# Performance work log

Hardware: AMD Instinct MI355X
Metric: run time of the kernel (lower is better)

## Reference

```python
import math
import jax, jax.numpy as jnp
import numpy as np

N = 50000      # nodes
E = 600000     # edges (before self-loops)
D_IN = 64
COND = 32
B = 50         # cond batch; N % B == 0
DT = 128       # dim_t
DH = 128       # dim_h
L = 3          # num GAT layers
FD = 16        # learned_sinusoidal_dim


def setup_inputs() -> dict:
    key = jax.random.key(0)
    ks = jax.random.split(key, 32)
    p = lambda k, shp: (jax.random.normal(k, shp, jnp.float32) * 0.05)
    return {
        "x": jax.random.normal(ks[0], (N, D_IN), jnp.float32),
        "adj": jax.random.randint(ks[1], (2, E), 0, N, dtype=jnp.int32),
        "ef": jax.random.normal(ks[2], (E, 8), jnp.float32),
        "timesteps": jax.random.uniform(ks[3], (N,), jnp.float32) * 1000.0,
        "cond": jax.random.normal(ks[4], (B, COND), jnp.float32),
        # random fourier weights (fixed, not trained in original since is_random=True)
        "fourier_w": jax.random.normal(ks[5], (FD // 2,), jnp.float32),
        # time MLP: Linear(FD+1, DT) -> SiLU -> Linear(DT, DT)
        "tW1": p(ks[6], (FD + 1, DT)), "tb1": p(ks[7], (DT,)),
        "tW2": p(ks[8], (DT, DT)),   "tb2": p(ks[9], (DT,)),
        # conditional projections
        "pxW": p(ks[10], (D_IN, DT)), "pxb": p(ks[11], (DT,)),
        "pcW": p(ks[12], (COND, DT)), "pcb": p(ks[13], (DT,)),
        # stacked GATConv params (all layers 128->128, heads=1)
        "linW": p(ks[14], (L, DT, DH)),   # lin, bias=False
        "attS": p(ks[15], (L, DH)),       # att_src
        "attD": p(ks[16], (L, DH)),       # att_dst
        "gbias": p(ks[17], (L, DH)),      # GATConv bias
        "resW": p(ks[18], (L, DT, DH)),   # residual Linear, bias=False
        # decode MLP
        "dW1": p(ks[19], (DH, DH)), "db1": p(ks[20], (DH,)),
        "dW2": p(ks[21], (DH, 2)),  "db2": p(ks[22], (2,)),
    }


def _gat_layer(h, src, dst, n, linW, attS, attD, gbias, resW):
    # PyG GATConv, heads=1, concat=True, residual=True, add_self_loops already in src/dst
    xl = h @ linW                          # [n, DH]
    a_src = xl @ attS                      # [n]
    a_dst = xl @ attD                      # [n]
    e = jax.nn.leaky_relu(a_src[src] + a_dst[dst], 0.2)   # [E2]
    m = jax.ops.segment_max(e, dst, num_segments=n)
    w = jnp.exp(e - m[dst])
    den = jax.ops.segment_sum(w, dst, num_segments=n)
    alpha = w / den[dst]                   # softmax per destination node
    out = jax.ops.segment_sum(alpha[:, None] * xl[src], dst, num_segments=n)
    return out + gbias + h @ resW


def reference(x, adj, ef, timesteps, cond, fourier_w, tW1, tb1, tW2, tb2,
              pxW, pxb, pcW, pcb, linW, attS, attD, gbias, resW,
              dW1, db1, dW2, db2):
    n = x.shape[0]
    # time embedding: random fourier features, dim = FD + 1
    t = timesteps[:, None]
    freqs = t * fourier_w[None, :] * (2.0 * math.pi)
    four = jnp.concatenate([t, jnp.sin(freqs), jnp.cos(freqs)], axis=-1)
    temb = jax.nn.silu(four @ tW1 + tb1) @ tW2 + tb2
    # conditional projection (cond repeated to match nodes)
    c = jnp.repeat(cond, n // cond.shape[0], axis=0)
    h = (x @ pxW + pxb) + (c @ pcW + pcb) + temb
    # add self-loops once (PyG GATConv default add_self_loops=True)
    loop = jnp.arange(n, dtype=adj.dtype)
    src = jnp.concatenate([adj[0], loop])
    dst = jnp.concatenate([adj[1], loop])
    for l in range(linW.shape[0]):
        h = _gat_layer(h, src, dst, n, linW[l], attS[l], attD[l], gbias[l], resW[l])
        h = jax.nn.gelu(h, approximate=False)
    # decode MLP
    h = jax.nn.gelu(h @ dW1 + db1, approximate=False)
    return h @ dW2 + db2
```

## Files before the change

kernel.cpp:

```cpp
#include <hip/hip_runtime.h>
#include <hip/hip_bf16.h>

#define N_NODES 50000
#define N_EDGES 600000
#define TOT_EDGES (N_EDGES + N_NODES)
#define NPB 1000
#define SCAN_BLK 49

#define PREP_T0 1563
#define PREP_T1 (PREP_T0 + 544)
#define PREP_T2 (PREP_T1 + 3125)
#define PREP_T3 (PREP_T2 + 25)
#define PREP_T4 (PREP_T3 + 3)

typedef __bf16 bf16x8 __attribute__((ext_vector_type(8)));
typedef float f32x4 __attribute__((ext_vector_type(4)));
typedef unsigned short u16x8 __attribute__((ext_vector_type(8)));

__device__ __forceinline__ float gelu_exact(float v){
  return 0.5f * v * (1.f + erff(v * 0.70710678118654752f));
}
__device__ __forceinline__ float silu(float v){
  return v / (1.f + expf(-v));
}
__device__ __forceinline__ unsigned short f2bf(float f){
  unsigned u = __builtin_bit_cast(unsigned, f);
  unsigned r = (u + 0x7FFFu + ((u >> 16) & 1u)) >> 16;
  return (unsigned short)r;
}
__device__ __forceinline__ float bf2f(unsigned short u){
  return __builtin_bit_cast(float, ((unsigned)u) << 16);
}

__global__ __launch_bounds__(256) void count_deg(const int* __restrict__ adj,
                                                 int* __restrict__ counts,
                                                 int* __restrict__ rank){
  int t = blockIdx.x*256 + threadIdx.x;
  if (t >= N_EDGES/4) return;
  int j4 = t*4;
  const int4 d4 = *(const int4*)&adj[N_EDGES + j4];
  int4 r4;
  r4.x = atomicAdd(&counts[d4.x], 1);
  r4.y = atomicAdd(&counts[d4.y], 1);
  r4.z = atomicAdd(&counts[d4.z], 1);
  r4.w = atomicAdd(&counts[d4.w], 1);
  *(int4*)&rank[j4] = r4;
}

__global__ __launch_bounds__(256) void scan_part(const int* __restrict__ counts, int* __restrict__ blksum){
  int tid = threadIdx.x;
  int base = blockIdx.x*1024 + tid*4;
  int s = 0;
  #pragma unroll
  for (int k = 0; k < 4; k++){ int idx = base+k; if (idx < N_NODES) s += counts[idx] + 1; }
  #pragma unroll
  for (int off = 1; off < 64; off <<= 1) s += __shfl_xor(s, off, 64);
  __shared__ int ws[4];
  int lane = tid & 63, wid = tid >> 6;
  if (lane == 0) ws[wid] = s;
  __syncthreads();
  if (tid == 0) blksum[blockIdx.x] = ws[0]+ws[1]+ws[2]+ws[3];
}

__global__ __launch_bounds__(256) void scan_final(const int* __restrict__ counts,
                                                  const int* __restrict__ blksum,
                                                  int* __restrict__ offsets,
                                                  int* __restrict__ srt_src){
  int tid = threadIdx.x; int lane = tid & 63, wid = tid >> 6;
  __shared__ int ws[4];
  __shared__ int sbase;
  int base = blockIdx.x*1024 + tid*4;
  int v[4]; int s = 0;
  #pragma unroll
  for (int k = 0; k < 4; k++){ int idx = base+k; v[k] = (idx < N_NODES) ? (counts[idx] + 1) : 0; s += v[k]; }
  int x = s;
  #pragma unroll
  for (int off = 1; off < 64; off <<= 1){
    int y = __shfl_up(x, off, 64);
    if (lane >= off) x += y;
  }
  if (lane == 63) ws[wid] = x;
  if (tid < 64){
    int bv = (tid < SCAN_BLK) ? blksum[tid] : 0;
    int bx = bv;
    #pragma unroll
    for (int off = 1; off < 64; off <<= 1){
      int y = __shfl_up(bx, off, 64);
      if (tid >= off) bx += y;
    }
    int basev = (blockIdx.x == 0) ? 0 : __shfl(bx, blockIdx.x - 1, 64);
    int total = __shfl(bx, SCAN_BLK - 1, 64);
    if (tid == 0){
      sbase = basev;
      if (blockIdx.x == SCAN_BLK-1) offsets[N_NODES] = total;
    }
  }
  __syncthreads();
  int run = sbase;
  for (int q = 0; q < wid; q++) run += ws[q];
  run += x - s;
  #pragma unroll
  for (int k = 0; k < 4; k++){
    int idx = base+k;
    if (idx < N_NODES){
      offsets[idx] = run;
      srt_src[run] = idx;
    }
    run += v[k];
  }
}

__global__ __launch_bounds__(256) void scatter_edges(const int* __restrict__ adj,
                                                     const int* __restrict__ rank,
                                                     const int* __restrict__ offsets,
                                                     int* __restrict__ srt_src){
  int t = blockIdx.x*256 + threadIdx.x;
  if (t >= N_EDGES/4) return;
  int j4 = t*4;
  const int4 s4 = *(const int4*)&adj[j4];
  const int4 d4 = *(const int4*)&adj[N_EDGES + j4];
  const int4 r4 = *(const int4*)&rank[j4];
  srt_src[offsets[d4.x] + 1 + r4.x] = s4.x;
  srt_src[offsets[d4.y] + 1 + r4.y] = s4.y;
  srt_src[offsets[d4.z] + 1 + r4.z] = s4.z;
  srt_src[offsets[d4.w] + 1 + r4.w] = s4.w;
}

__global__ __launch_bounds__(256) void prep_all(const float* __restrict__ timesteps,
                                                const float* __restrict__ fw,
                                                const float* __restrict__ tW1,
                                                const float* __restrict__ tb1,
                                                unsigned short* __restrict__ hid,
                                                const float* __restrict__ linW,
                                                const float* __restrict__ resW,
                                                const float* __restrict__ tW2,
                                                const float* __restrict__ pxW,
                                                const float* __restrict__ dW1,
                                                unsigned short* __restrict__ Bt2,
                                                unsigned short* __restrict__ Bt_init,
                                                unsigned short* __restrict__ Bt_d1,
                                                const float* __restrict__ x,
                                                unsigned short* __restrict__ xbf,
                                                const float* __restrict__ cond,
                                                const float* __restrict__ pcW,
                                                const float* __restrict__ pcb,
                                                float* __restrict__ cproj,
                                                const float* __restrict__ attS,
                                                const float* __restrict__ attD,
                                                float* __restrict__ uv){
  __shared__ float sfour[32][17];
  __shared__ float sW[17][128];
  const int bid = blockIdx.x, tid = threadIdx.x;

  if (bid < PREP_T0){
    int row0 = bid * 32;
    if (tid < 32){
      int gr = row0 + tid;
      float t = (gr < N_NODES) ? timesteps[gr] : 0.f;
      sfour[tid][0] = t;
      #pragma unroll
      for (int q = 0; q < 8; q++){
        float f = t * fw[q] * 6.2831853071795864769f;
        float sv, cv;
        sincosf(f, &sv, &cv);
        sfour[tid][1+q] = sv;
        sfour[tid][9+q] = cv;
      }
    }
    for (int i = tid; i < 17*128; i += 256) sW[i>>7][i&127] = tW1[i];
    __syncthreads();
    int j = tid & 127, rg = tid >> 7;
    float b = tb1[j];
    #pragma unroll
    for (int r = 0; r < 16; r++){
      int row = rg*16 + r;
      float acc = b;
      #pragma unroll
      for (int k = 0; k < 17; k++) acc += sfour[row][k]*sW[k][j];
      int gr = row0 + row;
      if (gr < N_NODES) hid[gr*128 + j] = f2bf(silu(acc));
    }
  } else if (bid < PREP_T1){
    int idx = (bid - PREP_T0)*256 + tid;
    if (idx < 98304){
      int j = idx >> 14, e = idx & 16383;
      int l = j >> 1, isres = j & 1;
      int k = e >> 7, c = e & 127;
      const float* src = (isres ? resW : linW) + l*16384;
      Bt2[(size_t)l*32768 + (size_t)(isres*128 + c)*128 + k] = f2bf(src[k*128 + c]);
    } else if (idx < 114688){
      int e = idx - 98304; int k = e >> 7, c = e & 127;
      Bt_init[c*192 + k] = f2bf(tW2[k*128 + c]);
    } else if (idx < 122880){
      int e = idx - 114688; int k = e >> 7, c = e & 127;
      Bt_init[c*192 + 128 + k] = f2bf(pxW[k*128 + c]);
    } else if (idx < 139264){
      int e = idx - 122880; int k = e >> 7, c = e & 127;
      Bt_d1[c*128 + k] = f2bf(dW1[k*128 + c]);
    }
  } else if (bid < PREP_T2){
    int i = (bid - PREP_T1)*256 + tid;
    float4 v = ((const float4*)x)[i];
    ushort4 o;
    o.x = f2bf(v.x); o.y = f2bf(v.y); o.z = f2bf(v.z); o.w = f2bf(v.w);
    *(ushort4*)&xbf[(size_t)i*4] = o;
  } else if (bid < PREP_T3){
    int g = (bid - PREP_T2)*256 + tid;
    int b = g >> 7, j = g & 127;
    float acc = pcb[j];
    for (int k = 0; k < 32; k++) acc += cond[b*32+k]*pcW[k*128+j];
    cproj[b*128+j] = acc;
  } else {
    int g = (bid - PREP_T3)*256 + tid;
    if (g < 768){
      int l = g >> 8, s = (g >> 7) & 1, k = g & 127;
      const float* att = s ? (attD + l*128) : (attS + l*128);
      const float* row = linW + (l*128 + k)*128;
      float acc = 0.f;
      for (int j = 0; j < 128; j++) acc += row[j]*att[j];
      uv[(l*2 + s)*128 + k] = acc;
    }
  }
}

template<int KD, int EPI, bool SWZ, bool DOTS>
__global__ __launch_bounds__(256) void mfma_gemm(const unsigned short* __restrict__ A0,
                                                 const unsigned short* __restrict__ A1,
                                                 const unsigned short* __restrict__ Bt,
                                                 const float* __restrict__ bias0,
                                                 const float* __restrict__ bias1,
                                                 const float* __restrict__ cproj,
                                                 unsigned short* __restrict__ O0,
                                                 unsigned short* __restrict__ O1,
                                                 const float* __restrict__ uv_l,
                                                 float* __restrict__ a_srcO,
                                                 float* __restrict__ a_dstO){
  constexpr int CHR  = KD / 8;
  constexpr int ROWB = KD * 2;
  constexpr int KS   = KD / 32;
  __shared__ alignas(16) char sA[64 * ROWB];
  const int tid  = threadIdx.x;
  int bx, nb;
  if constexpr (SWZ){
    int id = blockIdx.x;
    int nper = gridDim.x >> 3;
    int lin = (id & 7) * nper + (id >> 3);
    bx = lin >> 2; nb = lin & 3;
  } else {
    bx = blockIdx.x; nb = blockIdx.y;
  }
  const int m0   = bx * 64;
  const int lane = tid & 63, w = tid >> 6;
  const int lr   = lane & 15, lk = lane >> 4;

  bf16x8 bfr[4][KS];
  #pragma unroll
  for (int nt = 0; nt < 4; nt++){
    int c = nb*64 + nt*16 + lr;
    #pragma unroll
    for (int ks = 0; ks < KS; ks++)
      bfr[nt][ks] = *(const bf16x8*)&Bt[(size_t)c*KD + ks*32 + lk*8];
  }

  for (int i = tid; i < 64*CHR; i += 256){
    int r = i / CHR, ch = i % CHR;
    int grow = m0 + r;
    u16x8 v;
    #pragma unroll
    for (int q = 0; q < 8; q++) v[q] = 0;
    if (grow < N_NODES){
      if constexpr (KD == 128){
        v = *(const u16x8*)&A0[(size_t)grow*128 + ch*8];
      } else {
        if (ch < 16) v = *(const u16x8*)&A0[(size_t)grow*128 + ch*8];
        else         v = *(const u16x8*)&A1[(size_t)grow*64 + (ch-16)*8];
      }
    }
    *(u16x8*)&sA[r*ROWB + ((ch*16) ^ ((r & 7) << 4))] = v;
  }
  __syncthreads();

  f32x4 acc[4];
  #pragma unroll
  for (int nt = 0; nt < 4; nt++)
    #pragma unroll
    for (int q = 0; q < 4; q++) acc[nt][q] = 0.f;

  const int arow = w*16 + lr;
  #pragma unroll
  for (int ks = 0; ks < KS; ks++){
    bf16x8 a = *(const bf16x8*)&sA[arow*ROWB + ((ks*64 + lk*16) ^ ((arow & 7) << 4))];
    #pragma unroll
    for (int nt = 0; nt < 4; nt++)
      acc[nt] = __builtin_amdgcn_mfma_f32_16x16x32_bf16(a, bfr[nt][ks], acc[nt], 0, 0, 0);
  }

  if constexpr (DOTS){
    if (nb == 0){
      int r = tid >> 2;
      int row = m0 + r;
      if (row < N_NODES){
        float ps = 0.f, pd = 0.f;
        #pragma unroll
        for (int cc = 0; cc < 4; cc++){
          int ch = (tid & 3)*4 + cc;
          u16x8 av = *(const u16x8*)&sA[r*ROWB + ((ch*16) ^ ((r & 7) << 4))];
          int c0 = ch*8;
          const float4 u0 = *(const float4*)&uv_l[c0];
          const float4 u1 = *(const float4*)&uv_l[c0+4];
          const float4 v0 = *(const float4*)&uv_l[128+c0];
          const float4 v1 = *(const float4*)&uv_l[128+c0+4];
          const float uu[8] = {u0.x,u0.y,u0.z,u0.w,u1.x,u1.y,u1.z,u1.w};
          const float vv[8] = {v0.x,v0.y,v0.z,v0.w,v1.x,v1.y,v1.z,v1.w};
          #pragma unroll
          for (int q = 0; q < 8; q++){
            float hv = bf2f(av[q]);
            ps += hv*uu[q];
            pd += hv*vv[q];
          }
        }
        ps += __shfl_xor(ps, 1, 64); ps += __shfl_xor(ps, 2, 64);
        pd += __shfl_xor(pd, 1, 64); pd += __shfl_xor(pd, 2, 64);
        if ((tid & 3) == 0){ a_srcO[row] = ps; a_dstO[row] = pd; }
      }
    }
  }

  const int rbase = m0 + w*16 + lk*4;
  #pragma unroll
  for (int nt = 0; nt < 4; nt++){
    int c = nb*64 + nt*16 + lr;
    #pragma unroll
    for (int rg = 0; rg < 4; rg++){
      int row = rbase + rg;
      if (row >= N_NODES) continue;
      float v = acc[nt][rg];
      if constexpr (EPI == 0){
        if (c < 128) O0[(size_t)row*128 + c]       = f2bf(v);
        else         O1[(size_t)row*128 + (c-128)] = f2bf(v);
      } else if constexpr (EPI == 1){
        v += bias0[c] + bias1[c] + cproj[(row/NPB)*128 + c];
        O0[(size_t)row*128 + c] = f2bf(v);
      } else {
        v = gelu_exact(v + bias0[c]);
        O0[(size_t)row*128 + c] = f2bf(v);
      }
    }
  }
}

template<bool FUSE>
__global__ __launch_bounds__(256) void aggregate(const unsigned short* __restrict__ xl,
                                                 const float* __restrict__ a_src,
                                                 const float* __restrict__ a_dst,
                                                 const unsigned short* __restrict__ hres,
                                                 const float* __restrict__ gbias_l,
                                                 const int* __restrict__ offsets,
                                                 const int* __restrict__ srt_src,
                                                 unsigned short* __restrict__ h_out,
                                                 const float* __restrict__ uv_next,
                                                 float* __restrict__ a_src_o,
                                                 float* __restrict__ a_dst_o){
  const int tid  = threadIdx.x;
  const int lane = tid & 63;
  const int l16  = lane & 15;
  const int i    = blockIdx.x*16 + (tid >> 4);
  const int beg  = offsets[i];
  const int deg  = offsets[i+1] - beg;
  const float adst = a_dst[i];

  int   s0  = 0;
  float ev0 = -INFINITY;
  if (l16 < deg){
    s0 = srt_src[beg + l16];
    float t = a_src[s0] + adst;
    ev0 = (t > 0.f) ? t : 0.2f*t;
  }
  float m = ev0;
  #pragma unroll
  for (int off = 1; off < 16; off <<= 1) m = fmaxf(m, __shfl_xor(m, off, 64));
  float den = (l16 < deg) ? __expf(ev0 - m) : 0.f;
  #pragma unroll
  for (int off = 1; off < 16; off <<= 1) den += __shfl_xor(den, off, 64);
  for (int c0 = 16; c0 < deg; c0 += 16){
    float ev = -INFINITY;
    if (c0 + l16 < deg){
      int s = srt_src[beg + c0 + l16];
      float t = a_src[s] + adst;
      ev = (t > 0.f) ? t : 0.2f*t;
    }
    float cm = ev;
    #pragma unroll
    for (int off = 1; off < 16; off <<= 1) cm = fmaxf(cm, __shfl_xor(cm, off, 64));
    if (cm > m){ den *= __expf(m - cm); m = cm; }
    float wv = (c0 + l16 < deg) ? __expf(ev - m) : 0.f;
    #pragma unroll
    for (int off = 1; off < 16; off <<= 1) wv += __shfl_xor(wv, off, 64);
    den += wv;
  }
  const float inv = 1.f / den;
  float w0 = (l16 < deg) ? __expf(ev0 - m) * inv : 0.f;

  float acc[8];
  #pragma unroll
  for (int k = 0; k < 8; k++) acc[k] = 0.f;
  const int gbb = (lane & 48) << 2;

  int lim0 = deg < 16 ? deg : 16;
  for (int q = 0; q < lim0; q++){
    int addr = gbb + q*4;
    int s    = __builtin_amdgcn_ds_bpermute(addr, s0);
    float wq = __builtin_bit_cast(float, __builtin_amdgcn_ds_bpermute(addr, __builtin_bit_cast(int, w0)));
    const int4 xv = *(const int4*)&xl[((size_t)s << 7) + (l16 << 3)];
    const int xd[4] = {xv.x, xv.y, xv.z, xv.w};
    #pragma unroll
    for (int k = 0; k < 4; k++){
      acc[2*k]   += wq * __builtin_bit_cast(float, xd[k] << 16);
      acc[2*k+1] += wq * __builtin_bit_cast(float, xd[k] & 0xffff0000);
    }
  }
  for (int c0 = 16; c0 < deg; c0 += 16){
    int s1 = 0; float w1 = 0.f;
    if (c0 + l16 < deg){
      s1 = srt_src[beg + c0 + l16];
      float t = a_src[s1] + adst;
      float ev = (t > 0.f) ? t : 0.2f*t;
      w1 = __expf(ev - m) * inv;
    }
    int lim = deg - c0; if (lim > 16) lim = 16;
    for (int q = 0; q < lim; q++){
      int addr = gbb + q*4;
      int s    = __builtin_amdgcn_ds_bpermute(addr, s1);
      float wq = __builtin_bit_cast(float, __builtin_amdgcn_ds_bpermute(addr, __builtin_bit_cast(int, w1)));
      const int4 xv = *(const int4*)&xl[((size_t)s << 7) + (l16 << 3)];
      const int xd[4] = {xv.x, xv.y, xv.z, xv.w};
      #pragma unroll
      for (int k = 0; k < 4; k++){
        acc[2*k]   += wq * __builtin_bit_cast(float, xd[k] << 16);
        acc[2*k+1] += wq * __builtin_bit_cast(float, xd[k] & 0xffff0000);
      }
    }
  }

  const int4 hr = *(const int4*)&hres[((size_t)i << 7) + (l16 << 3)];
  const int hd[4] = {hr.x, hr.y, hr.z, hr.w};
  const float4 gb0 = *(const float4*)&gbias_l[l16*8];
  const float4 gb1 = *(const float4*)&gbias_l[l16*8 + 4];
  const float gbv[8] = {gb0.x, gb0.y, gb0.z, gb0.w, gb1.x, gb1.y, gb1.z, gb1.w};
  float uu[8], vv[8];
  if constexpr (FUSE){
    const float4 a0 = *(const float4*)&uv_next[l16*8];
    const float4 a1 = *(const float4*)&uv_next[l16*8 + 4];
    const float4 b0 = *(const float4*)&uv_next[128 + l16*8];
    const float4 b1 = *(const float4*)&uv_next[128 + l16*8 + 4];
    uu[0]=a0.x; uu[1]=a0.y; uu[2]=a0.z; uu[3]=a0.w; uu[4]=a1.x; uu[5]=a1.y; uu[6]=a1.z; uu[7]=a1.w;
    vv[0]=b0.x; vv[1]=b0.y; vv[2]=b0.z; vv[3]=b0.w; vv[4]=b1.x; vv[5]=b1.y; vv[6]=b1.z; vv[7]=b1.w;
  }
  float ps = 0.f, pd = 0.f;
  int od[4];
  #pragma unroll
  for (int k = 0; k < 4; k++){
    float r0 = acc[2*k]   + gbv[2*k]   + __builtin_bit_cast(float, hd[k] << 16);
    float r1 = acc[2*k+1] + gbv[2*k+1] + __builtin_bit_cast(float, hd[k] & 0xffff0000);
    float g0 = gelu_exact(r0);
    float g1 = gelu_exact(r1);
    if constexpr (FUSE){
      ps += g0*uu[2*k] + g1*uu[2*k+1];
      pd += g0*vv[2*k] + g1*vv[2*k+1];
    }
    unsigned lo = f2bf(g0);
    unsigned hi = f2bf(g1);
    od[k] = (int)(lo | (hi << 16));
  }
  *(int4*)&h_out[((size_t)i << 7) + (l16 << 3)] = make_int4(od[0], od[1], od[2], od[3]);
  if constexpr (FUSE){
    #pragma unroll
    for (int off = 1; off < 16; off <<= 1){
      ps += __shfl_xor(ps, off, 64);
      pd += __shfl_xor(pd, off, 64);
    }
    if (l16 == 0){ a_src_o[i] = ps; a_dst_o[i] = pd; }
  }
}

__global__ __launch_bounds__(256) void head2(const unsigned short* __restrict__ g,
                                             const float* __restrict__ dW2,
                                             const float* __restrict__ db2,
                                             float* __restrict__ out){
  const int tid = threadIdx.x;
  const int l16 = tid & 15;
  const int i   = blockIdx.x*16 + (tid >> 4);
  const int4 gv = *(const int4*)&g[((size_t)i << 7) + (l16 << 3)];
  const int gd[4] = {gv.x, gv.y, gv.z, gv.w};
  float wk[16];
  #pragma unroll
  for (int q = 0; q < 4; q++){
    const float4 wq = *(const float4*)&dW2[l16*16 + q*4];
    wk[q*4+0]=wq.x; wk[q*4+1]=wq.y; wk[q*4+2]=wq.z; wk[q*4+3]=wq.w;
  }
  float p0 = 0.f, p1 = 0.f;
  #pragma unroll
  for (int k = 0; k < 4; k++){
    float lo = __builtin_bit_cast(float, gd[k] << 16);
    float hi = __builtin_bit_cast(float, gd[k] & 0xffff0000);
    p0 += lo*wk[4*k+0] + hi*wk[4*k+2];
    p1 += lo*wk[4*k+1] + hi*wk[4*k+3];
  }
  #pragma unroll
  for (int off = 1; off < 16; off <<= 1){
    p0 += __shfl_xor(p0, off, 64);
    p1 += __shfl_xor(p1, off, 64);
  }
  if (l16 == 0){
    float2 o; o.x = p0 + db2[0]; o.y = p1 + db2[1];
    *(float2*)&out[i*2] = o;
  }
}

extern "C" void kernel_launch(void* const* d_in, const int* in_sizes, int n_in,
                              void* d_out, int out_size, void* d_ws, size_t ws_size,
                              hipStream_t stream) {
  const float* x   = (const float*)d_in[0];
  const int*   adj = (const int*)  d_in[1];
  const float* timesteps = (const float*)d_in[3];
  const float* cond = (const float*)d_in[4];
  const float* fw   = (const float*)d_in[5];
  const float* tW1  = (const float*)d_in[6];
  const float* tb1  = (const float*)d_in[7];
  const float* tW2  = (const float*)d_in[8];
  const float* tb2  = (const float*)d_in[9];
  const float* pxW  = (const float*)d_in[10];
  const float* pxb  = (const float*)d_in[11];
  const float* pcW  = (const float*)d_in[12];
  const float* pcb  = (const float*)d_in[13];
  const float* linW = (const float*)d_in[14];
  const float* attS = (const float*)d_in[15];
  const float* attD = (const float*)d_in[16];
  const float* gbias= (const float*)d_in[17];
  const float* resW = (const float*)d_in[18];
  const float* dW1  = (const float*)d_in[19];
  const float* db1  = (const float*)d_in[20];
  const float* dW2  = (const float*)d_in[21];
  const float* db2  = (const float*)d_in[22];
  float* out = (float*)d_out;

  char* w = (char*)d_ws;
  size_t off = 0;
  auto carve = [&](size_t bytes) -> void* {
    void* p = w + off;
    off = (off + bytes + 255) & ~(size_t)255;
    return p;
  };
  unsigned short* h_bf    = (unsigned short*)carve((size_t)N_NODES*128*2);
  unsigned short* xl_bf   = (unsigned short*)carve((size_t)N_NODES*128*2);
  unsigned short* hres_bf = (unsigned short*)carve((size_t)N_NODES*128*2);
  unsigned short* x_bf    = (unsigned short*)carve((size_t)N_NODES*64*2);
  float* a_src0 = (float*)carve((size_t)N_NODES*4);
  float* a_dst0 = (float*)carve((size_t)N_NODES*4);
  float* a_src1 = (float*)carve((size_t)N_NODES*4);
  float* a_dst1 = (float*)carve((size_t)N_NODES*4);
  float* cproj = (float*)carve(50*128*4);
  float* uv    = (float*)carve(6*128*4);
  int* counts  = (int*)carve((size_t)N_NODES*4);
  int* rank    = (int*)carve((size_t)N_EDGES*4);
  int* offsets = (int*)carve((size_t)(N_NODES+1)*4);
  int* srt_src = (int*)carve((size_t)TOT_EDGES*4);
  int* blksum  = (int*)carve(SCAN_BLK*4);
  unsigned short* Bt2     = (unsigned short*)carve((size_t)3*256*128*2);
  unsigned short* Bt_init = (unsigned short*)carve((size_t)128*192*2);
  unsigned short* Bt_d1   = (unsigned short*)carve((size_t)128*128*2);
  (void)ws_size; (void)in_sizes; (void)n_in; (void)out_size;

  const int edge4_blocks = (N_EDGES/4 + 255)/256;
  const int gemm_gx      = (N_NODES + 63)/64;
  const int grp_blocks   = N_NODES/16;

  hipMemsetAsync(counts, 0, (size_t)N_NODES*4, stream);
  count_deg<<<edge4_blocks, 256, 0, stream>>>(adj, counts, rank);
  scan_part<<<SCAN_BLK, 256, 0, stream>>>(counts, blksum);
  scan_final<<<SCAN_BLK, 256, 0, stream>>>(counts, blksum, offsets, srt_src);
  scatter_edges<<<edge4_blocks, 256, 0, stream>>>(adj, rank, offsets, srt_src);

  prep_all<<<PREP_T4, 256, 0, stream>>>(timesteps, fw, tW1, tb1, xl_bf ,
                                        linW, resW, tW2, pxW, dW1, Bt2, Bt_init, Bt_d1,
                                        x, x_bf, cond, pcW, pcb, cproj, attS, attD, uv);

  mfma_gemm<192,1,false,false><<<dim3(gemm_gx,2), 256, 0, stream>>>(xl_bf , x_bf, Bt_init, tb2, pxb, cproj, h_bf, nullptr, nullptr, nullptr, nullptr);

  float* asrc_in = a_src0; float* adst_in = a_dst0;
  float* asrc_out = a_src1; float* adst_out = a_dst1;
  for (int l = 0; l < 3; l++){
    if (l == 0){
      mfma_gemm<128,0,true,true><<<gemm_gx*4, 256, 0, stream>>>(h_bf, nullptr, Bt2, nullptr, nullptr, nullptr, xl_bf, hres_bf, uv, asrc_in, adst_in);
    } else {
      mfma_gemm<128,0,true,false><<<gemm_gx*4, 256, 0, stream>>>(h_bf, nullptr, Bt2 + (size_t)l*32768, nullptr, nullptr, nullptr, xl_bf, hres_bf, nullptr, nullptr, nullptr);
    }
    if (l < 2){
      aggregate<true><<<grp_blocks, 256, 0, stream>>>(xl_bf, asrc_in, adst_in, hres_bf, gbias + l*128,
                                                      offsets, srt_src, h_bf, uv + (l+1)*256, asrc_out, adst_out);
      float* t0 = asrc_in; asrc_in = asrc_out; asrc_out = t0;
      float* t1 = adst_in; adst_in = adst_out; adst_out = t1;
    } else {
      aggregate<false><<<grp_blocks, 256, 0, stream>>>(xl_bf, asrc_in, adst_in, hres_bf, gbias + l*128,
                                                       offsets, srt_src, h_bf, nullptr, nullptr, nullptr);
    }
  }

  mfma_gemm<128,2,false,false><<<dim3(gemm_gx,2), 256, 0, stream>>>(h_bf, nullptr, Bt_d1, db1, nullptr, nullptr, xl_bf , nullptr, nullptr, nullptr, nullptr);
  head2<<<grp_blocks, 256, 0, stream>>>(xl_bf , dW2, db2, out);
}
```

Measured before the change: 462.9 us.

## Compute full output width per GEMM block with weights staged in LDS

The GEMM kernel no longer splits output columns across blocks. Each block now loads its 64-row A tile once and computes all NC columns (128 or 256), staging the weight matrix in shared memory instead of per-wave registers. This drops the redundant A-tile loads across column blocks and the block-index swizzle. In exchange, each block needs more LDS (up to 64KB for KD=128, NC=256), there are fewer blocks, and every block reloads the full weight matrix, which may lower occupancy.

Measured after the change: 409.7 us. 1.13x faster.

```diff
diff --git a/kernel.cpp b/kernel.cpp
--- a/kernel.cpp
+++ b/kernel.cpp
@@ -223,7 +223,7 @@
   }
 }
 
-template<int KD, int EPI, bool SWZ, bool DOTS>
+template<int KD, int NC, int EPI, bool DOTS>
 __global__ __launch_bounds__(256) void mfma_gemm(const unsigned short* __restrict__ A0,
                                                  const unsigned short* __restrict__ A1,
                                                  const unsigned short* __restrict__ Bt,
@@ -238,29 +238,13 @@
   constexpr int CHR  = KD / 8;
   constexpr int ROWB = KD * 2;
   constexpr int KS   = KD / 32;
+  constexpr int NT   = NC / 16;
   __shared__ alignas(16) char sA[64 * ROWB];
+  __shared__ alignas(16) char sB[NC * ROWB];
   const int tid  = threadIdx.x;
-  int bx, nb;
-  if constexpr (SWZ){
-    int id = blockIdx.x;
-    int nper = gridDim.x >> 3;
-    int lin = (id & 7) * nper + (id >> 3);
-    bx = lin >> 2; nb = lin & 3;
-  } else {
-    bx = blockIdx.x; nb = blockIdx.y;
-  }
-  const int m0   = bx * 64;
+  const int m0   = blockIdx.x * 64;
   const int lane = tid & 63, w = tid >> 6;
   const int lr   = lane & 15, lk = lane >> 4;
-
-  bf16x8 bfr[4][KS];
-  #pragma unroll
-  for (int nt = 0; nt < 4; nt++){
-    int c = nb*64 + nt*16 + lr;
-    #pragma unroll
-    for (int ks = 0; ks < KS; ks++)
-      bfr[nt][ks] = *(const bf16x8*)&Bt[(size_t)c*KD + ks*32 + lk*8];
-  }
 
   for (int i = tid; i < 64*CHR; i += 256){
     int r = i / CHR, ch = i % CHR;
@@ -278,58 +262,68 @@
     }
     *(u16x8*)&sA[r*ROWB + ((ch*16) ^ ((r & 7) << 4))] = v;
   }
+  for (int i = tid; i < NC*CHR; i += 256){
+    int r = i / CHR, ch = i % CHR;
+    u16x8 v = *(const u16x8*)&Bt[(size_t)r*KD + ch*8];
+    *(u16x8*)&sB[r*ROWB + ((ch*16) ^ ((r & 7) << 4))] = v;
+  }
   __syncthreads();
 
-  f32x4 acc[4];
-  #pragma unroll
-  for (int nt = 0; nt < 4; nt++)
+  bf16x8 afr[KS];
+  const int arow = w*16 + lr;
+  #pragma unroll
+  for (int ks = 0; ks < KS; ks++)
+    afr[ks] = *(const bf16x8*)&sA[arow*ROWB + ((ks*64 + lk*16) ^ ((arow & 7) << 4))];
+
+  f32x4 acc[NT];
+  #pragma unroll
+  for (int nt = 0; nt < NT; nt++)
     #pragma unroll
     for (int q = 0; q < 4; q++) acc[nt][q] = 0.f;
 
-  const int arow = w*16 + lr;
-  #pragma unroll
-  for (int ks = 0; ks < KS; ks++){
-    bf16x8 a = *(const bf16x8*)&sA[arow*ROWB + ((ks*64 + lk*16) ^ ((arow & 7) << 4))];
-    #pragma unroll
-    for (int nt = 0; nt < 4; nt++)
-      acc[nt] = __builtin_amdgcn_mfma_f32_16x16x32_bf16(a, bfr[nt][ks], acc[nt], 0, 0, 0);
+  #pragma unroll
+  for (int nt = 0; nt < NT; nt++){
+    const int brow = nt*16 + lr;
+    #pragma unroll
+    for (int ks = 0; ks < KS; ks++){
+      bf16x8 b = *(const bf16x8*)&sB[brow*ROWB + ((ks*64 + lk*16) ^ ((brow & 7) << 4))];
+      acc[nt] = __builtin_amdgcn_mfma_f32_16x16x32_bf16(afr[ks], b, acc[nt], 0, 0, 0);
+    }
   }
 
   if constexpr (DOTS){
-    if (nb == 0){
-      int r = tid >> 2;
-      int row = m0 + r;
-      if (row < N_NODES){
-        float ps = 0.f, pd = 0.f;
+    int r = tid >> 2;
+    int row = m0 + r;
+    if (row < N_NODES){
+      float ps = 0.f, pd = 0.f;
+      #pragma unroll
+      for (int cc = 0; cc < 4; cc++){
+        int ch = (tid & 3)*4 + cc;
+        u16x8 av = *(const u16x8*)&sA[r*ROWB + ((ch*16) ^ ((r & 7) << 4))];
+        int c0 = ch*8;
+        const float4 u0 = *(const float4*)&uv_l[c0];
+        const float4 u1 = *(const float4*)&uv_l[c0+4];
+        const float4 v0 = *(const float4*)&uv_l[128+c0];
+        const float4 v1 = *(const float4*)&uv_l[128+c0+4];
+        const float uu[8] = {u0.x,u0.y,u0.z,u0.w,u1.x,u1.y,u1.z,u1.w};
+        const float vv[8] = {v0.x,v0.y,v0.z,v0.w,v1.x,v1.y,v1.z,v1.w};
         #pragma unroll
-        for (int cc = 0; cc < 4; cc++){
-          int ch = (tid & 3)*4 + cc;
-          u16x8 av = *(const u16x8*)&sA[r*ROWB + ((ch*16) ^ ((r & 7) << 4))];
-          int c0 = ch*8;
-          const float4 u0 = *(const float4*)&uv_l[c0];
-          const float4 u1 = *(const float4*)&uv_l[c0+4];
-          const float4 v0 = *(const float4*)&uv_l[128+c0];
-          const float4 v1 = *(const float4*)&uv_l[128+c0+4];
-          const float uu[8] = {u0.x,u0.y,u0.z,u0.w,u1.x,u1.y,u1.z,u1.w};
-          const float vv[8] = {v0.x,v0.y,v0.z,v0.w,v1.x,v1.y,v1.z,v1.w};
-          #pragma unroll
-          for (int q = 0; q < 8; q++){
-            float hv = bf2f(av[q]);
-            ps += hv*uu[q];
-            pd += hv*vv[q];
-          }
+        for (int q = 0; q < 8; q++){
+          float hv = bf2f(av[q]);
+          ps += hv*uu[q];
+          pd += hv*vv[q];
         }
-        ps += __shfl_xor(ps, 1, 64); ps += __shfl_xor(ps, 2, 64);
-        pd += __shfl_xor(pd, 1, 64); pd += __shfl_xor(pd, 2, 64);
-        if ((tid & 3) == 0){ a_srcO[row] = ps; a_dstO[row] = pd; }
       }
+      ps += __shfl_xor(ps, 1, 64); ps += __shfl_xor(ps, 2, 64);
+      pd += __shfl_xor(pd, 1, 64); pd += __shfl_xor(pd, 2, 64);
+      if ((tid & 3) == 0){ a_srcO[row] = ps; a_dstO[row] = pd; }
     }
   }
 
   const int rbase = m0 + w*16 + lk*4;
   #pragma unroll
-  for (int nt = 0; nt < 4; nt++){
-    int c = nb*64 + nt*16 + lr;
+  for (int nt = 0; nt < NT; nt++){
+    int c = nt*16 + lr;
     #pragma unroll
     for (int rg = 0; rg < 4; rg++){
       int row = rbase + rg;
@@ -585,15 +579,15 @@
                                         linW, resW, tW2, pxW, dW1, Bt2, Bt_init, Bt_d1,
                                         x, x_bf, cond, pcW, pcb, cproj, attS, attD, uv);
 
-  mfma_gemm<192,1,false,false><<<dim3(gemm_gx,2), 256, 0, stream>>>(xl_bf , x_bf, Bt_init, tb2, pxb, cproj, h_bf, nullptr, nullptr, nullptr, nullptr);
+  mfma_gemm<192,128,1,false><<<gemm_gx, 256, 0, stream>>>(xl_bf , x_bf, Bt_init, tb2, pxb, cproj, h_bf, nullptr, nullptr, nullptr, nullptr);
 
   float* asrc_in = a_src0; float* adst_in = a_dst0;
   float* asrc_out = a_src1; float* adst_out = a_dst1;
   for (int l = 0; l < 3; l++){
     if (l == 0){
-      mfma_gemm<128,0,true,true><<<gemm_gx*4, 256, 0, stream>>>(h_bf, nullptr, Bt2, nullptr, nullptr, nullptr, xl_bf, hres_bf, uv, asrc_in, adst_in);
+      mfma_gemm<128,256,0,true><<<gemm_gx, 256, 0, stream>>>(h_bf, nullptr, Bt2, nullptr, nullptr, nullptr, xl_bf, hres_bf, uv, asrc_in, adst_in);
     } else {
-      mfma_gemm<128,0,true,false><<<gemm_gx*4, 256, 0, stream>>>(h_bf, nullptr, Bt2 + (size_t)l*32768, nullptr, nullptr, nullptr, xl_bf, hres_bf, nullptr, nullptr, nullptr);
+      mfma_gemm<128,256,0,false><<<gemm_gx, 256, 0, stream>>>(h_bf, nullptr, Bt2 + (size_t)l*32768, nullptr, nullptr, nullptr, xl_bf, hres_bf, nullptr, nullptr, nullptr);
     }
     if (l < 2){
       aggregate<true><<<grp_blocks, 256, 0, stream>>>(xl_bf, asrc_in, adst_in, hres_bf, gbias + l*128,
@@ -606,6 +600,6 @@
     }
   }
 
-  mfma_gemm<128,2,false,false><<<dim3(gemm_gx,2), 256, 0, stream>>>(h_bf, nullptr, Bt_d1, db1, nullptr, nullptr, xl_bf , nullptr, nullptr, nullptr, nullptr);
+  mfma_gemm<128,128,2,false><<<gemm_gx, 256, 0, stream>>>(h_bf, nullptr, Bt_d1, db1, nullptr, nullptr, xl_bf , nullptr, nullptr, nullptr, nullptr);
   head2<<<grp_blocks, 256, 0, stream>>>(xl_bf , dW2, db2, out);
 }
```
